# Kernel tuning notes

Measured on AMD Instinct MI355X. Metric: run time of the kernel, lower is better.

Reference implementation:

```python
import jax, jax.numpy as jnp
import numpy as np
from jax import lax

BN_EPS = 1e-3  # keras BatchNormalization default epsilon
TOP_K = 2      # keep_top_k


def _conv3(x, k, b, s):
    # x: NDHWC, k: DHWIO, 'SAME' padding like keras Conv3D(padding='same')
    y = lax.conv_general_dilated(x, k, (s, s, s), 'SAME',
                                 dimension_numbers=('NDHWC', 'DHWIO', 'NDHWC'))
    return y + b


def _bn(x, g, be, m, v):
    # inference-mode batch norm with moving statistics
    return g * (x - m) * lax.rsqrt(v + BN_EPS) + be


def setup_inputs() -> dict:
    key = jax.random.key(0)
    ks = jax.random.split(key, 64)
    B, S = 16, 96
    nf, ksz, nE, nb = 32, 3, 8, 4
    inp = {"x": jax.random.normal(ks[0], (B, S, S, S, 1), jnp.float32)}
    cin = 1
    for i in range(nb):
        cout = nf * 2 ** i
        base = 1 + 6 * i
        inp["k%d" % i] = jax.random.normal(ks[base], (ksz, ksz, ksz, cin, cout), jnp.float32) * 0.05
        inp["b%d" % i] = jnp.zeros((cout,), jnp.float32)
        inp["g%d" % i] = 1.0 + 0.1 * jax.random.normal(ks[base + 1], (cout,), jnp.float32)
        inp["be%d" % i] = 0.1 * jax.random.normal(ks[base + 2], (cout,), jnp.float32)
        inp["m%d" % i] = 0.1 * jax.random.normal(ks[base + 3], (cout,), jnp.float32)
        inp["v%d" % i] = jax.random.uniform(ks[base + 4], (cout,), jnp.float32, 0.5, 1.5)
        cin = cout
    c = nf * 2 ** (nb - 1)  # 256
    inp["w1k"] = jax.random.normal(ks[30], (1, 1, 1, c, c), jnp.float32) * 0.05
    inp["w1b"] = jnp.zeros((c,), jnp.float32)
    inp["wg"] = 1.0 + 0.1 * jax.random.normal(ks[31], (c,), jnp.float32)
    inp["wbe"] = 0.1 * jax.random.normal(ks[32], (c,), jnp.float32)
    inp["wm"] = 0.1 * jax.random.normal(ks[33], (c,), jnp.float32)
    inp["wv"] = jax.random.uniform(ks[34], (c,), jnp.float32, 0.5, 1.5)
    inp["w2k"] = jax.random.normal(ks[35], (1, 1, 1, c, nE), jnp.float32) * 0.05
    inp["w2b"] = jnp.zeros((nE,), jnp.float32)
    return inp


def reference(x, k0, b0, g0, be0, m0, v0, k1, b1, g1, be1, m1, v1,
              k2, b2, g2, be2, m2, v2, k3, b3, g3, be3, m3, v3,
              w1k, w1b, wg, wbe, wm, wv, w2k, w2b):
    blocks = [(k0, b0, g0, be0, m0, v0), (k1, b1, g1, be1, m1, v1),
              (k2, b2, g2, be2, m2, v2), (k3, b3, g3, be3, m3, v3)]
    h = x
    for k, b, g, be, m, v in blocks:  # EncoderBlock: Conv3D(stride 2)+BN+ReLU
        h = jax.nn.relu(_bn(_conv3(h, k, b, 2), g, be, m, v))
    h = jnp.mean(h, axis=(1, 2, 3), keepdims=True)  # GAP, [B,1,1,1,256]
    w = _conv3(h, w1k, w1b, 1)
    w = jax.nn.relu(_bn(w, wg, wbe, wm, wv))
    w = _conv3(w, w2k, w2b, 1)  # [B,1,1,1,n_experts]
    # noisy-top-k gating (noise disabled at inference): mask non-top-k to -inf
    top_vals = lax.top_k(w, TOP_K)[0]
    thr = top_vals[..., TOP_K - 1:TOP_K]
    w = jnp.where(w >= thr, w, -jnp.inf)
    return jax.nn.softmax(w, axis=-1)
```

## Files before the change

kernel.cpp:

```cpp
#include <hip/hip_runtime.h>
#include <math.h>

#define BN_EPS 1e-3f

typedef __attribute__((ext_vector_type(8))) unsigned short ushort8v;
typedef __attribute__((ext_vector_type(8))) short short8v;
typedef __attribute__((ext_vector_type(4))) float f32x4;
typedef __attribute__((ext_vector_type(4))) unsigned int uint4v;

__device__ __forceinline__ float4 f4load(const float* p) {
    return *reinterpret_cast<const float4*>(p);
}
__device__ __forceinline__ float bf2f(unsigned short u) {
    union { unsigned int i; float f; } w; w.i = ((unsigned int)u) << 16; return w.f;
}
__device__ __forceinline__ unsigned short f2bf(float f) {
    union { float fv; unsigned int i; } w; w.fv = f;
    unsigned int lsb = (w.i >> 16) & 1u;
    w.i += 0x7fffu + lsb;
    return (unsigned short)(w.i >> 16);
}
__device__ __forceinline__ unsigned cvtpk(float lo, float hi) {
    unsigned r;
    asm("v_cvt_pk_bf16_f32 %0, %1, %2" : "=v"(r) : "v"(lo), "v"(hi));
    return r;
}
template<int N> __device__ __forceinline__ void waitv() {
    asm volatile("s_waitcnt vmcnt(%0)" :: "n"(N) : "memory");
}

#define GLOAD_LDS16(g, l)                                                     \
    __builtin_amdgcn_global_load_lds(                                         \
        (const __attribute__((address_space(1))) void*)(const void*)(g),      \
        (__attribute__((address_space(3))) void*)(void*)(l), 16, 0, 0)

template<int CIN, int COUT>
__device__ __forceinline__ void wprep_body(
    const float* __restrict__ k, unsigned short* __restrict__ wt, int blk)
{
    constexpr int NS = COUT / 16;
    constexpr int KS = CIN / 32;
    int idx = blk * 256 + (int)threadIdx.x;
    if (idx >= 27 * KS * NS * 64) return;
    int lane = idx & 63;
    int nsg  = (idx >> 6) % NS;
    int it   = idx / (64 * NS);
    int tap  = it / KS;
    int ks   = it - tap * KS;
    int sg = lane >> 4, lr = lane & 15;
    int cout = nsg * 16 + lr;
    ushort8v o;
    #pragma unroll
    for (int j = 0; j < 8; ++j) {
        int ci = ks * 32 + sg * 8 + j;
        o[j] = f2bf(k[(size_t)(tap * CIN + ci) * COUT + cout]);
    }
    *reinterpret_cast<ushort8v*>(wt + (size_t)idx * 8) = o;
}

__global__ __launch_bounds__(256) void wprep_all(
    const float* __restrict__ k0,
    const float* __restrict__ k1, const float* __restrict__ k2, const float* __restrict__ k3,
    unsigned short* __restrict__ w0f,
    unsigned short* __restrict__ w1, unsigned short* __restrict__ w2, unsigned short* __restrict__ w3,
    unsigned short* __restrict__ zp)
{
    int b = blockIdx.x;
    if (b < 27)       wprep_body<32, 64>(k1, w1, b);
    else if (b < 135) wprep_body<64, 128>(k2, w2, b - 27);
    else if (b < 567) wprep_body<128, 256>(k3, w3, b - 135);
    else {
        reinterpret_cast<unsigned int*>(zp)[threadIdx.x] = 0u;
        {
            int t = (int)threadIdx.x;
            int lane = t & 63;
            int mf = (t >> 6) & 1;
            int ns = t >> 7;
            int sg = lane >> 4, lr = lane & 15;
            ushort8v o;
            #pragma unroll
            for (int j = 0; j < 8; ++j) {
                int jj = mf * 8 + j;
                bool valid = (sg < 3) && (jj < 9);
                int tap = sg * 9 + jj;
                o[j] = valid ? f2bf(k0[tap * 32 + ns * 16 + lr]) : (unsigned short)0;
            }
            *reinterpret_cast<ushort8v*>(w0f + (size_t)t * 8) = o;
        }
    }
}

__global__ __launch_bounds__(256) void conv0_lds(
    const float* __restrict__ x, const unsigned short* __restrict__ w0f,
    const float* __restrict__ zf,
    const float* __restrict__ b, const float* __restrict__ g,
    const float* __restrict__ be, const float* __restrict__ m,
    const float* __restrict__ v, unsigned short* __restrict__ y)
{
    __shared__ __attribute__((aligned(16))) float tile[81 * 36];

    const int l   = threadIdx.x & 63;
    const int wid = threadIdx.x >> 6;
    const int sg  = l >> 4;
    const int lr  = l & 15;

    int bb = blockIdx.x;
    const int owt = bb % 3;  bb /= 3;
    const int oht = bb % 12; bb /= 12;
    const int odt = bb % 12; const int n = bb / 12;

    const int id0 = odt * 8, ih0 = oht * 8, iw0 = owt * 32;

    #pragma unroll
    for (int q0 = 0; q0 < 729; q0 += 256) {
        int qq = q0 + wid * 64;
        int q  = qq + l;
        if (qq < 729 && q < 729) {
            int row = q / 9, c = q - row * 9;
            int dd = row / 9, hh = row - dd * 9;
            int id = id0 + dd, ih = ih0 + hh;
            const float* src =
                (id < 96 && ih < 96 && (c < 8 || iw0 + 32 < 96))
                ? x + ((size_t)(n * 96 + id) * 96 + ih) * 96 + iw0 + c * 4
                : zf;
            GLOAD_LDS16(src, (char*)tile + (size_t)qq * 16);
        }
    }
    __syncthreads();

    const short8v B00 = *(const short8v*)(w0f + (size_t)(0 * 64 + l) * 8);
    const short8v B01 = *(const short8v*)(w0f + (size_t)(1 * 64 + l) * 8);
    const short8v B10 = *(const short8v*)(w0f + (size_t)(2 * 64 + l) * 8);
    const short8v B11 = *(const short8v*)(w0f + (size_t)(3 * 64 + l) * 8);

    float rc[9][3];
    {
        int dcl = (sg < 3) ? (2 * wid + sg) : 0;
        const float* rb = tile + (size_t)(dcl * 9) * 36 + 2 * lr;
        #pragma unroll
        for (int r = 0; r < 9; ++r) {
            float2 lo = *reinterpret_cast<const float2*>(rb + r * 36);
            rc[r][0] = lo.x; rc[r][1] = lo.y;
            rc[r][2] = rb[r * 36 + 2];
        }
    }

    f32x4 acc[4][2];
    #pragma unroll
    for (int mi = 0; mi < 4; ++mi) {
        acc[mi][0] = (f32x4){0.f, 0.f, 0.f, 0.f};
        acc[mi][1] = (f32x4){0.f, 0.f, 0.f, 0.f};
    }

    #pragma unroll
    for (int mi = 0; mi < 4; ++mi) {
        const int h0 = 2 * mi;
        uint4v au0;
        au0[0] = cvtpk(rc[h0][0],     rc[h0][1]);
        au0[1] = cvtpk(rc[h0][2],     rc[h0 + 1][0]);
        au0[2] = cvtpk(rc[h0 + 1][1], rc[h0 + 1][2]);
        au0[3] = cvtpk(rc[h0 + 2][0], rc[h0 + 2][1]);
        short8v a0 = __builtin_bit_cast(short8v, au0);
        uint4v au1;
        au1[0] = cvtpk(rc[h0 + 2][2], 0.f);
        au1[1] = 0; au1[2] = 0; au1[3] = 0;
        short8v a1 = __builtin_bit_cast(short8v, au1);
        acc[mi][0] = __builtin_amdgcn_mfma_f32_16x16x32_bf16(B00, a0, acc[mi][0], 0, 0, 0);
        acc[mi][0] = __builtin_amdgcn_mfma_f32_16x16x32_bf16(B01, a1, acc[mi][0], 0, 0, 0);
        acc[mi][1] = __builtin_amdgcn_mfma_f32_16x16x32_bf16(B10, a0, acc[mi][1], 0, 0, 0);
        acc[mi][1] = __builtin_amdgcn_mfma_f32_16x16x32_bf16(B11, a1, acc[mi][1], 0, 0, 0);
    }

    float4 Sv[2], Tv[2];
    #pragma unroll
    for (int ns = 0; ns < 2; ++ns) {
        int c0 = ns * 16 + sg * 4;
        float4 gv = f4load(g + c0), vv = f4load(v + c0);
        float4 bv = f4load(b + c0), mv = f4load(m + c0), bev = f4load(be + c0);
        Sv[ns].x = gv.x * rsqrtf(vv.x + BN_EPS);
        Sv[ns].y = gv.y * rsqrtf(vv.y + BN_EPS);
        Sv[ns].z = gv.z * rsqrtf(vv.z + BN_EPS);
        Sv[ns].w = gv.w * rsqrtf(vv.w + BN_EPS);
        Tv[ns].x = (bv.x - mv.x) * Sv[ns].x + bev.x;
        Tv[ns].y = (bv.y - mv.y) * Sv[ns].y + bev.y;
        Tv[ns].z = (bv.z - mv.z) * Sv[ns].z + bev.z;
        Tv[ns].w = (bv.w - mv.w) * Sv[ns].w + bev.w;
    }
    const int odG = odt * 4 + wid;
    const int owG = owt * 16 + lr;
    #pragma unroll
    for (int mi = 0; mi < 4; ++mi) {
        int oh = oht * 4 + mi;
        unsigned short* yp =
            y + (((size_t)(n * 48 + odG) * 48 + oh) * 48 + owG) * 32;
        #pragma unroll
        for (int ns = 0; ns < 2; ++ns) {
            float v0 = fmaxf(acc[mi][ns][0] * Sv[ns].x + Tv[ns].x, 0.f);
            float v1 = fmaxf(acc[mi][ns][1] * Sv[ns].y + Tv[ns].y, 0.f);
            float v2 = fmaxf(acc[mi][ns][2] * Sv[ns].z + Tv[ns].z, 0.f);
            float v3 = fmaxf(acc[mi][ns][3] * Sv[ns].w + Tv[ns].w, 0.f);
            uint2 uu;
            uu.x = cvtpk(v0, v1);
            uu.y = cvtpk(v2, v3);
            *reinterpret_cast<uint2*>(yp + ns * 16 + sg * 4) = uu;
        }
    }
}

template<int CIN, int COUT, int INS, int OUTS, int MW, int NSW, int NH,
         int CSPLIT, int KU>
__global__ __launch_bounds__(256, 2) void conv_mfma_lds(
    const unsigned short* __restrict__ x, const unsigned short* __restrict__ wt,
    const unsigned short* __restrict__ zp,
    const float* __restrict__ b, const float* __restrict__ g,
    const float* __restrict__ be, const float* __restrict__ m,
    const float* __restrict__ v, unsigned short* __restrict__ y)
{
    constexpr int NSfull = COUT / 16;
    constexpr int NSB = NSW * NH;
    constexpr int KS = CIN / 32;
    constexpr int NITK = 27 * KS;
    constexpr int NIT = NITK / KU;
    constexpr int MGROUPS = 4 / NH;
    constexpr int MTILE = MGROUPS * MW * 16;
    constexpr int BSTEP = NSB * KU * 1024;
    constexpr int ASTEP = MGROUPS * MW * KU * 1024;
    constexpr int STRIDE = BSTEP + ASTEP;
    constexpr int BL = (NSB * KU) / 4;
    constexpr int AL = MW * KU;
    static_assert(NSB * CSPLIT == NSfull && NITK % KU == 0 && (NSB * KU) % 4 == 0, "tiling");
    static_assert(NIT >= 3, "pipeline depth");

    __shared__ __attribute__((aligned(16))) char lds[3 * STRIDE];

    const int l   = threadIdx.x & 63;
    const int wid = threadIdx.x >> 6;
    const int sg  = l >> 4;
    const int lr  = l & 15;

    const int mblk   = blockIdx.x / CSPLIT;
    const int cchunk = blockIdx.x % CSPLIT;
    const int mgroup = wid / NH;
    const int ngroup = wid % NH;
    const int gCoutBase = (cchunk * NSB + ngroup * NSW) * 16;
    const int vwave = mblk * MTILE + mgroup * MW * 16;

    const int vvS = l >> 2;
    const int ssS = ((l & 3) - (l >> 3)) & 3;

    const unsigned short* ap0[MW];
    unsigned smask[MW];
    #pragma unroll
    for (int mi = 0; mi < MW; ++mi) {
        int vA = vwave + mi * 16 + vvS;
        int owA = vA % OUTS; int t1 = vA / OUTS;
        int ohA = t1 % OUTS; int t2 = t1 / OUTS;
        int odA = t2 % OUTS; int nA = t2 / OUTS;
        ap0[mi] = x + ((((size_t)nA * INS + 2 * odA) * INS + 2 * ohA) * INS + 2 * owA) * CIN + ssS * 8;
        smask[mi] = ((odA == OUTS - 1) ? 0x07FC0000u : 0u)
                  | ((ohA == OUTS - 1) ? 0x070381C0u : 0u)
                  | ((owA == OUTS - 1) ? 0x04924924u : 0u);
    }

    const unsigned short* zpl = (const unsigned short*)((const char*)zp + l * 16);
    const int slotA = (lr * 4 + ((sg + (lr >> 1)) & 3)) * 16;

    f32x4 acc[MW][NSW];
    #pragma unroll
    for (int mi = 0; mi < MW; ++mi)
        #pragma unroll
        for (int ns = 0; ns < NSW; ++ns) acc[mi][ns] = (f32x4){0.f, 0.f, 0.f, 0.f};

    auto stage = [&](int ito, int p) {
        char* dst = &lds[p * STRIDE];
        #pragma unroll
        for (int c = 0; c < BL; ++c) {
            int idx  = c * 256 + (int)threadIdx.x;
            int lane = idx & 63;
            int sub  = idx >> 6;
            int u    = sub / NSB;
            int grp  = sub % NSB;
            int it   = ito * KU + u;
            const unsigned short* src =
                wt + ((size_t)(it * NSfull + cchunk * NSB + grp) * 64 + lane) * 8;
            GLOAD_LDS16(src, dst + sub * 1024);
        }
        if (ngroup == 0) {
            #pragma unroll
            for (int u = 0; u < KU; ++u) {
                int it = ito * KU + u;
                int tap = (KS == 1) ? it : it / KS;
                int ks  = (KS == 1) ? 0  : it - tap * KS;
                int kd = tap / 9, r9 = tap - kd * 9, kh = r9 / 3, kw = r9 - kh * 3;
                size_t aoff = (size_t)((kd * INS + kh) * INS + kw) * CIN + ks * 32;
                #pragma unroll
                for (int mi = 0; mi < MW; ++mi) {
                    const unsigned short* ga =
                        ((smask[mi] >> tap) & 1u) ? zpl : (ap0[mi] + aoff);
                    GLOAD_LDS16(ga, dst + BSTEP + ((mgroup * MW + mi) * KU + u) * 1024);
                }
            }
        }
    };

    auto computestep = [&](const char* buf) {
        #pragma unroll
        for (int u = 0; u < KU; ++u) {
            short8v Bf[NSW], Af[MW];
            #pragma unroll
            for (int ns = 0; ns < NSW; ++ns)
                Bf[ns] = *(const short8v*)(buf + (u * NSB + ngroup * NSW + ns) * 1024 + l * 16);
            #pragma unroll
            for (int mi = 0; mi < MW; ++mi)
                Af[mi] = *(const short8v*)(buf + BSTEP + ((mgroup * MW + mi) * KU + u) * 1024 + slotA);
            #pragma unroll
            for (int mi = 0; mi < MW; ++mi)
                #pragma unroll
                for (int ns = 0; ns < NSW; ++ns)
                    acc[mi][ns] = __builtin_amdgcn_mfma_f32_16x16x32_bf16(Bf[ns], Af[mi], acc[mi][ns], 0, 0, 0);
        }
    };

    stage(0, 0);
    stage(1, 1);
    #pragma unroll 1
    for (int ito = 0; ito < NIT - 1; ++ito) {
        if (ngroup == 0) waitv<BL + AL>(); else waitv<BL>();
        __builtin_amdgcn_s_barrier();
        asm volatile("" ::: "memory");
        if (ito + 2 < NIT) stage(ito + 2, (ito + 2) % 3);
        computestep(&lds[(ito % 3) * STRIDE]);
    }
    waitv<0>();
    __builtin_amdgcn_s_barrier();
    asm volatile("" ::: "memory");
    computestep(&lds[((NIT - 1) % 3) * STRIDE]);

    float4 Sv[NSW], Tv[NSW];
    #pragma unroll
    for (int ns = 0; ns < NSW; ++ns) {
        int c0 = gCoutBase + ns * 16 + sg * 4;
        float4 gv = f4load(g + c0), vv = f4load(v + c0);
        float4 bv = f4load(b + c0), mv = f4load(m + c0), bev = f4load(be + c0);
        Sv[ns].x = gv.x * rsqrtf(vv.x + BN_EPS);
        Sv[ns].y = gv.y * rsqrtf(vv.y + BN_EPS);
        Sv[ns].z = gv.z * rsqrtf(vv.z + BN_EPS);
        Sv[ns].w = gv.w * rsqrtf(vv.w + BN_EPS);
        Tv[ns].x = (bv.x - mv.x) * Sv[ns].x + bev.x;
        Tv[ns].y = (bv.y - mv.y) * Sv[ns].y + bev.y;
        Tv[ns].z = (bv.z - mv.z) * Sv[ns].z + bev.z;
        Tv[ns].w = (bv.w - mv.w) * Sv[ns].w + bev.w;
    }
    #pragma unroll
    for (int mi = 0; mi < MW; ++mi) {
        int vD = vwave + mi * 16 + lr;
        int ow = vD % OUTS; int u1 = vD / OUTS;
        int oh = u1 % OUTS; int u2 = u1 / OUTS;
        int od = u2 % OUTS; int n = u2 / OUTS;
        unsigned short* yp =
            y + ((((size_t)n * OUTS + od) * OUTS + oh) * OUTS + ow) * COUT + gCoutBase;
        #pragma unroll
        for (int ns = 0; ns < NSW; ++ns) {
            float v0 = fmaxf(acc[mi][ns][0] * Sv[ns].x + Tv[ns].x, 0.f);
            float v1 = fmaxf(acc[mi][ns][1] * Sv[ns].y + Tv[ns].y, 0.f);
            float v2 = fmaxf(acc[mi][ns][2] * Sv[ns].z + Tv[ns].z, 0.f);
            float v3 = fmaxf(acc[mi][ns][3] * Sv[ns].w + Tv[ns].w, 0.f);
            uint2 uu;
            uu.x = cvtpk(v0, v1);
            uu.y = cvtpk(v2, v3);
            *reinterpret_cast<uint2*>(yp + ns * 16 + sg * 4) = uu;
        }
    }
}

__global__ __launch_bounds__(256) void head_kernel(
    const unsigned short* __restrict__ x4,
    const float* __restrict__ w1k, const float* __restrict__ w1b,
    const float* __restrict__ wg,  const float* __restrict__ wbe,
    const float* __restrict__ wm,  const float* __restrict__ wv,
    const float* __restrict__ w2k, const float* __restrict__ w2b,
    float* __restrict__ out)
{
    __shared__ float part[8][256];
    __shared__ float h[256];
    __shared__ float r[256];
    __shared__ float logits[8];

    const int n = blockIdx.x;
    const int t = threadIdx.x;
    const int c8 = t & 31;
    const int pg = t >> 5;

    const unsigned short* xb = x4 + (size_t)n * 216 * 256 + c8 * 8;
    float s[8] = {0.f, 0.f, 0.f, 0.f, 0.f, 0.f, 0.f, 0.f};
    for (int i = pg; i < 216; i += 8) {
        ushort8v v8 = *reinterpret_cast<const ushort8v*>(xb + (size_t)i * 256);
        #pragma unroll
        for (int j = 0; j < 8; ++j) s[j] += bf2f(v8[j]);
    }
    #pragma unroll
    for (int j = 0; j < 8; ++j) part[pg][c8 * 8 + j] = s[j];
    __syncthreads();

    float a = 0.f;
    #pragma unroll
    for (int gi = 0; gi < 8; ++gi) a += part[gi][t];
    h[t] = a * (1.0f / 216.0f);
    __syncthreads();

    float acc = w1b[t];
    #pragma unroll 4
    for (int ci = 0; ci < 256; ++ci) acc += h[ci] * w1k[ci * 256 + t];
    float sc = wg[t] * rsqrtf(wv[t] + BN_EPS);
    acc = (acc - wm[t]) * sc + wbe[t];
    r[t] = fmaxf(acc, 0.f);
    __syncthreads();

    if (t < 8) {
        float a2 = w2b[t];
        for (int ci = 0; ci < 256; ++ci) a2 += r[ci] * w2k[ci * 8 + t];
        logits[t] = a2;
    }
    __syncthreads();

    if (t == 0) {
        float m1 = -INFINITY, m2 = -INFINITY;
        for (int e = 0; e < 8; ++e) {
            float val = logits[e];
            if (val > m1) { m2 = m1; m1 = val; }
            else if (val > m2) { m2 = val; }
        }
        float thr = m2;
        float ex[8]; float sum = 0.f;
        for (int e = 0; e < 8; ++e) {
            float val = (logits[e] >= thr) ? logits[e] : -INFINITY;
            ex[e] = expf(val - m1);
            sum += ex[e];
        }
        float inv = 1.0f / sum;
        for (int e = 0; e < 8; ++e) out[n * 8 + e] = ex[e] * inv;
    }
}

extern "C" void kernel_launch(void* const* d_in, const int* in_sizes, int n_in,
                              void* d_out, int out_size, void* d_ws, size_t ws_size,
                              hipStream_t stream) {
    const float* x   = (const float*)d_in[0];
    const float* k0  = (const float*)d_in[1];
    const float* b0  = (const float*)d_in[2];
    const float* g0  = (const float*)d_in[3];
    const float* be0 = (const float*)d_in[4];
    const float* m0  = (const float*)d_in[5];
    const float* v0  = (const float*)d_in[6];
    const float* k1  = (const float*)d_in[7];
    const float* b1  = (const float*)d_in[8];
    const float* g1  = (const float*)d_in[9];
    const float* be1 = (const float*)d_in[10];
    const float* m1  = (const float*)d_in[11];
    const float* v1  = (const float*)d_in[12];
    const float* k2  = (const float*)d_in[13];
    const float* b2  = (const float*)d_in[14];
    const float* g2  = (const float*)d_in[15];
    const float* be2 = (const float*)d_in[16];
    const float* m2  = (const float*)d_in[17];
    const float* v2  = (const float*)d_in[18];
    const float* k3  = (const float*)d_in[19];
    const float* b3  = (const float*)d_in[20];
    const float* g3  = (const float*)d_in[21];
    const float* be3 = (const float*)d_in[22];
    const float* m3  = (const float*)d_in[23];
    const float* v3  = (const float*)d_in[24];
    const float* w1k = (const float*)d_in[25];
    const float* w1b = (const float*)d_in[26];
    const float* wg  = (const float*)d_in[27];
    const float* wbe = (const float*)d_in[28];
    const float* wm  = (const float*)d_in[29];
    const float* wv  = (const float*)d_in[30];
    const float* w2k = (const float*)d_in[31];
    const float* w2b = (const float*)d_in[32];

    unsigned short* x1  = (unsigned short*)d_ws;
    unsigned short* x2  = x1 + 56623104;
    unsigned short* x3  = x2 + 14155776;
    unsigned short* x4  = x3 + 3538944;
    unsigned short* Wt1 = x4 + 884736;
    unsigned short* Wt2 = Wt1 + 55296;
    unsigned short* Wt3 = Wt2 + 221184;
    unsigned short* zp  = Wt3 + 884736;
    unsigned short* W0f = zp + 512;

    wprep_all<<<568, 256, 0, stream>>>(k0, k1, k2, k3, W0f, Wt1, Wt2, Wt3, zp);
    conv0_lds<<<6912, 256, 0, stream>>>(x, W0f, (const float*)zp, b0, g0, be0, m0, v0, x1);
    conv_mfma_lds<32, 64, 48, 24, 2, 4, 1, 1, 1><<<1728, 256, 0, stream>>>(x1, Wt1, zp, b1, g1, be1, m1, v1, x2);
    conv_mfma_lds<64, 128, 24, 12, 1, 4, 2, 1, 1><<<864, 256, 0, stream>>>(x2, Wt2, zp, b2, g2, be2, m2, v2, x3);
    conv_mfma_lds<128, 256, 12, 6, 1, 1, 4, 4, 2><<<864, 256, 0, stream>>>(x3, Wt3, zp, b3, g3, be3, m3, v3, x4);
    head_kernel<<<16, 256, 0, stream>>>(x4, w1k, w1b, wg, wbe, wm, wv, w2k, w2b, (float*)d_out);
}
```

Baseline: 184.8 us.

## Load conv weights directly to registers, deepen LDS activation pipeline

Weight (B) fragments are now loaded from global memory straight into registers with double-buffered register arrays, instead of being staged through LDS. LDS is used only for activation tiles, and that pipeline is deepened from 3 to 4 buffers. The aim is to cut LDS traffic and capacity for weights and hide more global latency. In exchange, when several waves share the same weights they each fetch them separately from global memory or cache, register pressure rises, and the waitcnt accounting becomes more fragile.

```diff
diff --git a/kernel.cpp b/kernel.cpp
--- a/kernel.cpp
+++ b/kernel.cpp
@@ -209,7 +209,7 @@
 
 template<int CIN, int COUT, int INS, int OUTS, int MW, int NSW, int NH,
          int CSPLIT, int KU>
-__global__ __launch_bounds__(256, 2) void conv_mfma_lds(
+__global__ __launch_bounds__(256, 2) void conv_mfma_bg(
     const unsigned short* __restrict__ x, const unsigned short* __restrict__ wt,
     const unsigned short* __restrict__ zp,
     const float* __restrict__ b, const float* __restrict__ g,
@@ -223,15 +223,13 @@
     constexpr int NIT = NITK / KU;
     constexpr int MGROUPS = 4 / NH;
     constexpr int MTILE = MGROUPS * MW * 16;
-    constexpr int BSTEP = NSB * KU * 1024;
     constexpr int ASTEP = MGROUPS * MW * KU * 1024;
-    constexpr int STRIDE = BSTEP + ASTEP;
-    constexpr int BL = (NSB * KU) / 4;
     constexpr int AL = MW * KU;
-    static_assert(NSB * CSPLIT == NSfull && NITK % KU == 0 && (NSB * KU) % 4 == 0, "tiling");
-    static_assert(NIT >= 3, "pipeline depth");
-
-    __shared__ __attribute__((aligned(16))) char lds[3 * STRIDE];
+    constexpr int BF = NSW * KU;
+    static_assert(NSB * CSPLIT == NSfull && NITK % KU == 0, "tiling");
+    static_assert(NIT >= 5, "pipeline depth");
+
+    __shared__ __attribute__((aligned(16))) char lds[4 * ASTEP];
 
     const int l   = threadIdx.x & 63;
     const int wid = threadIdx.x >> 6;
@@ -242,6 +240,7 @@
     const int cchunk = blockIdx.x % CSPLIT;
     const int mgroup = wid / NH;
     const int ngroup = wid % NH;
+    const bool stager = (ngroup == 0);
     const int gCoutBase = (cchunk * NSB + ngroup * NSW) * 16;
     const int vwave = mblk * MTILE + mgroup * MW * 16;
 
@@ -271,70 +270,102 @@
         #pragma unroll
         for (int ns = 0; ns < NSW; ++ns) acc[mi][ns] = (f32x4){0.f, 0.f, 0.f, 0.f};
 
-    auto stage = [&](int ito, int p) {
-        char* dst = &lds[p * STRIDE];
-        #pragma unroll
-        for (int c = 0; c < BL; ++c) {
-            int idx  = c * 256 + (int)threadIdx.x;
-            int lane = idx & 63;
-            int sub  = idx >> 6;
-            int u    = sub / NSB;
-            int grp  = sub % NSB;
-            int it   = ito * KU + u;
-            const unsigned short* src =
-                wt + ((size_t)(it * NSfull + cchunk * NSB + grp) * 64 + lane) * 8;
-            GLOAD_LDS16(src, dst + sub * 1024);
-        }
-        if (ngroup == 0) {
+    auto astage = [&](int ito, int p) {
+        if (!stager) return;
+        char* dst = &lds[p * ASTEP];
+        #pragma unroll
+        for (int u = 0; u < KU; ++u) {
+            int it = ito * KU + u;
+            int tap = (KS == 1) ? it : it / KS;
+            int ks  = (KS == 1) ? 0  : it - tap * KS;
+            int kd = tap / 9, r9 = tap - kd * 9, kh = r9 / 3, kw = r9 - kh * 3;
+            size_t aoff = (size_t)((kd * INS + kh) * INS + kw) * CIN + ks * 32;
             #pragma unroll
-            for (int u = 0; u < KU; ++u) {
+            for (int mi = 0; mi < MW; ++mi) {
+                const unsigned short* ga =
+                    ((smask[mi] >> tap) & 1u) ? zpl : (ap0[mi] + aoff);
+                GLOAD_LDS16(ga, dst + ((mgroup * MW + mi) * KU + u) * 1024);
+            }
+        }
+    };
+
+    auto bload = [&](int ito, short8v (&B)[BF]) {
+        #pragma unroll
+        for (int u = 0; u < KU; ++u)
+            #pragma unroll
+            for (int ns = 0; ns < NSW; ++ns) {
                 int it = ito * KU + u;
-                int tap = (KS == 1) ? it : it / KS;
-                int ks  = (KS == 1) ? 0  : it - tap * KS;
-                int kd = tap / 9, r9 = tap - kd * 9, kh = r9 / 3, kw = r9 - kh * 3;
-                size_t aoff = (size_t)((kd * INS + kh) * INS + kw) * CIN + ks * 32;
-                #pragma unroll
-                for (int mi = 0; mi < MW; ++mi) {
-                    const unsigned short* ga =
-                        ((smask[mi] >> tap) & 1u) ? zpl : (ap0[mi] + aoff);
-                    GLOAD_LDS16(ga, dst + BSTEP + ((mgroup * MW + mi) * KU + u) * 1024);
-                }
+                B[u * NSW + ns] = *(const short8v*)(
+                    wt + ((size_t)(it * NSfull + cchunk * NSB + ngroup * NSW + ns) * 64 + l) * 8);
             }
-        }
     };
 
-    auto computestep = [&](const char* buf) {
+    auto computestep = [&](int ito, short8v (&B)[BF]) {
+        const char* buf = &lds[(ito & 3) * ASTEP];
         #pragma unroll
         for (int u = 0; u < KU; ++u) {
-            short8v Bf[NSW], Af[MW];
-            #pragma unroll
-            for (int ns = 0; ns < NSW; ++ns)
-                Bf[ns] = *(const short8v*)(buf + (u * NSB + ngroup * NSW + ns) * 1024 + l * 16);
+            short8v Af[MW];
             #pragma unroll
             for (int mi = 0; mi < MW; ++mi)
-                Af[mi] = *(const short8v*)(buf + BSTEP + ((mgroup * MW + mi) * KU + u) * 1024 + slotA);
+                Af[mi] = *(const short8v*)(buf + ((mgroup * MW + mi) * KU + u) * 1024 + slotA);
             #pragma unroll
             for (int mi = 0; mi < MW; ++mi)
                 #pragma unroll
                 for (int ns = 0; ns < NSW; ++ns)
-                    acc[mi][ns] = __builtin_amdgcn_mfma_f32_16x16x32_bf16(Bf[ns], Af[mi], acc[mi][ns], 0, 0, 0);
+                    acc[mi][ns] = __builtin_amdgcn_mfma_f32_16x16x32_bf16(B[u * NSW + ns], Af[mi], acc[mi][ns], 0, 0, 0);
         }
     };
 
-    stage(0, 0);
-    stage(1, 1);
+    short8v Bc[BF], Bn[BF];
+
+    bload(0, Bc);
+    astage(0, 0);
+    astage(1, 1);
+    astage(2, 2);
+
+    if (stager) waitv<2 * AL>();
+    __builtin_amdgcn_s_barrier();
+    asm volatile("" ::: "memory");
+    astage(3, 3);
+    bload(1, Bn);
+    computestep(0, Bc);
+
+    if (stager) waitv<2 * AL + BF>();
+    __builtin_amdgcn_s_barrier();
+    asm volatile("" ::: "memory");
+    if (4 < NIT) astage(4, 0);
+    bload(2, Bc);
+    computestep(1, Bn);
+
+    int it = 2;
     #pragma unroll 1
-    for (int ito = 0; ito < NIT - 1; ++ito) {
-        if (ngroup == 0) waitv<BL + AL>(); else waitv<BL>();
+    for (; it + 1 < NIT - 1; it += 2) {
+        if (stager) waitv<2 * AL + 2 * BF>();
         __builtin_amdgcn_s_barrier();
         asm volatile("" ::: "memory");
-        if (ito + 2 < NIT) stage(ito + 2, (ito + 2) % 3);
-        computestep(&lds[(ito % 3) * STRIDE]);
+        if (it + 3 < NIT) astage(it + 3, (it + 3) & 3);
+        bload(it + 1, Bn);
+        computestep(it, Bc);
+        if (stager) waitv<2 * AL + 2 * BF>();
+        __builtin_amdgcn_s_barrier();
+        asm volatile("" ::: "memory");
+        if (it + 4 < NIT) astage(it + 4, (it + 4) & 3);
+        bload(it + 2, Bc);
+        computestep(it + 1, Bn);
+    }
+    if (it < NIT - 1) {
+        if (stager) waitv<2 * AL + 2 * BF>();
+        __builtin_amdgcn_s_barrier();
+        asm volatile("" ::: "memory");
+        bload(it + 1, Bn);
+        computestep(it, Bc);
+        ++it;
     }
     waitv<0>();
     __builtin_amdgcn_s_barrier();
     asm volatile("" ::: "memory");
-    computestep(&lds[((NIT - 1) % 3) * STRIDE]);
+    if constexpr (((NIT - 1) & 1) == 0) computestep(NIT - 1, Bc);
+    else                                computestep(NIT - 1, Bn);
 
     float4 Sv[NSW], Tv[NSW];
     #pragma unroll
@@ -491,8 +522,8 @@
 
     wprep_all<<<568, 256, 0, stream>>>(k0, k1, k2, k3, W0f, Wt1, Wt2, Wt3, zp);
     conv0_lds<<<6912, 256, 0, stream>>>(x, W0f, (const float*)zp, b0, g0, be0, m0, v0, x1);
-    conv_mfma_lds<32, 64, 48, 24, 2, 4, 1, 1, 1><<<1728, 256, 0, stream>>>(x1, Wt1, zp, b1, g1, be1, m1, v1, x2);
-    conv_mfma_lds<64, 128, 24, 12, 1, 4, 2, 1, 1><<<864, 256, 0, stream>>>(x2, Wt2, zp, b2, g2, be2, m2, v2, x3);
-    conv_mfma_lds<128, 256, 12, 6, 1, 1, 4, 4, 2><<<864, 256, 0, stream>>>(x3, Wt3, zp, b3, g3, be3, m3, v3, x4);
+    conv_mfma_bg<32, 64, 48, 24, 2, 4, 1, 1, 1><<<1728, 256, 0, stream>>>(x1, Wt1, zp, b1, g1, be1, m1, v1, x2);
+    conv_mfma_bg<64, 128, 24, 12, 1, 4, 2, 1, 1><<<864, 256, 0, stream>>>(x2, Wt2, zp, b2, g2, be2, m2, v2, x3);
+    conv_mfma_bg<128, 256, 12, 6, 1, 1, 4, 4, 2><<<864, 256, 0, stream>>>(x3, Wt3, zp, b3, g3, be3, m3, v3, x4);
     head_kernel<<<16, 256, 0, stream>>>(x4, w1k, w1b, wg, wbe, wm, wv, w2k, w2b, (float*)d_out);
 }
```

After: 203.5 us. 10.1% more time.
